# Kernel optimization log

Measured on AMD Instinct MI355X. Metric: run time of the kernel, lower is better.

The kernel has to match this reference:

```python
import jax, jax.numpy as jnp
import numpy as np

N_NODES = 10000
N_EDGES = 320000
K_HOPS = 3
IN_CH = 128
OUT_CH = 128


def setup_inputs() -> dict:
    key = jax.random.key(0)
    k1, k2, k3, k4, k5 = jax.random.split(key, 5)
    h = jax.random.normal(k1, (N_NODES, IN_CH), dtype=jnp.float32)
    X = jax.random.normal(k2, (N_EDGES, K_HOPS), dtype=jnp.float32)
    edge_index = jax.random.randint(k3, (2, N_EDGES), 0, N_NODES, dtype=jnp.int64)
    batch_node = jax.random.uniform(k4, (N_NODES,), dtype=jnp.float32)
    # glorot init for weight, zeros for bias (matches reset_parameters)
    stdv = np.sqrt(6.0 / (IN_CH + OUT_CH))
    weight = jax.random.uniform(k5, (K_HOPS, IN_CH, OUT_CH), dtype=jnp.float32,
                                minval=-stdv, maxval=stdv)
    bias = jnp.zeros((OUT_CH,), dtype=jnp.float32)
    return {"h": h, "X": X, "edge_index": edge_index,
            "batch_node": batch_node, "weight": weight, "bias": bias}


def reference(h, X, edge_index, batch_node, weight, bias):
    # Original builds dense A[k, src, dst] = X[e, k] (zeros elsewhere), then
    # res = A @ h @ weight, max over k, + bias. We honor the sparsity:
    # agg[src, k, :] = sum_e X[e, k] * h[dst[e], :]  (sparse A @ h per hop k)
    n = batch_node.shape[0]
    src = edge_index[0]
    dst = edge_index[1]
    msg = X[:, :, None] * h[dst][:, None, :]                 # [E, K, in]
    agg = jax.ops.segment_sum(msg, src, num_segments=n)      # [N, K, in]
    res = jnp.einsum('nki,kio->kno', agg, weight)            # [K, N, out]
    out = res.max(axis=0) + bias                             # [N, out]
    return out
```

## Files before the change

### kernel.cpp

```cpp
#include <hip/hip_runtime.h>

#define N_NODES 10000
#define N_EDGES 320000
#define K_HOPS  3
#define CH      128
#define NPB     16
#define NGRP    (N_NODES / NPB)
#define CAP     80
#define BCAP    768
#define GSTRIDE 64
#define ROWP    136

#define EDGE_BLKS 1250
#define WCV_BLKS  192

typedef __attribute__((ext_vector_type(8))) short  frag8;
typedef __attribute__((ext_vector_type(4))) float  floatx4;

__device__ inline unsigned short f2bf(float x) {
    union { float f; unsigned u; } v; v.f = x;
    unsigned r = v.u + 0x7fff + ((v.u >> 16) & 1);
    return (unsigned short)(r >> 16);
}
__device__ inline unsigned pack2bf(float lo, float hi) {
    return (unsigned)f2bf(lo) | ((unsigned)f2bf(hi) << 16);
}

__global__ __launch_bounds__(256) void bin_kernel(
    const int* __restrict__ ei, const float* __restrict__ W,
    unsigned short* __restrict__ WT, int* __restrict__ gcur,
    unsigned* __restrict__ bstore)
{
    int b = blockIdx.x;
    if (b < EDGE_BLKS) {
        int e   = b * 256 + threadIdx.x;
        int src = ei[e];
        int grp = src >> 4;
        int nl  = src & 15;
        int r = atomicAdd(gcur + grp * GSTRIDE, 1);
        if (r < BCAP)
            bstore[(size_t)grp * BCAP + r] = (unsigned)e | ((unsigned)nl << 20);
    } else {
        int tid = (b - EDGE_BLKS) * 256 + threadIdx.x;
        int i = tid & 127;
        int o = (tid >> 7) & 127;
        int k = tid >> 14;
        WT[tid] = f2bf(W[((size_t)k * CH + i) * CH + o]);
    }
}

__global__ __launch_bounds__(512) void fused_kernel(
    const float*          __restrict__ h,
    const float*          __restrict__ X,
    const int*            __restrict__ ei,
    const int*            __restrict__ gcur,
    const unsigned*       __restrict__ bstore,
    const unsigned short* __restrict__ WT,
    const float*          __restrict__ bias,
    float*                __restrict__ out)
{
    __shared__ unsigned short sA[K_HOPS][NPB][ROWP];
    __shared__ unsigned sEl[NPB][CAP];
    __shared__ int      cur[NPB];
    const int b     = blockIdx.x;
    const int node0 = b * NPB;
    const int t = threadIdx.x, w = t >> 6, lane = t & 63;

    if (t < NPB) cur[t] = 0;
    __syncthreads();

    {
        const int cnt = min(gcur[b * GSTRIDE], BCAP);
        const unsigned* bp = bstore + (size_t)b * BCAP;
        for (int i = t; i < cnt; i += 512) {
            unsigned pk = bp[i];
            int nl = (int)(pk >> 20);
            int r = atomicAdd(&cur[nl], 1);
            if (r < CAP) sEl[nl][r] = pk & 0xFFFFFu;
        }
    }
    __syncthreads();

    const int cb = 2 * lane;
#pragma unroll
    for (int q = 0; q < 2; ++q) {
        const int nl = 2 * w + q;
        const int cnt = __builtin_amdgcn_readfirstlane(min(cur[nl], CAP));
        const unsigned* lst = sEl[nl];
        float a0 = 0.f, a1 = 0.f, a2 = 0.f, a3 = 0.f, a4 = 0.f, a5 = 0.f;

        const int full = cnt & ~7;
        for (int s = 0; s < full; s += 8) {
            int e[8], dst[8]; float x0[8], x1[8], x2[8]; float2 hv[8];
#pragma unroll
            for (int k = 0; k < 8; ++k) e[k] = (int)lst[s + k];
#pragma unroll
            for (int k = 0; k < 8; ++k) dst[k] = ei[N_EDGES + e[k]];
#pragma unroll
            for (int k = 0; k < 8; ++k) {
                x0[k] = X[3 * e[k]]; x1[k] = X[3 * e[k] + 1]; x2[k] = X[3 * e[k] + 2];
            }
#pragma unroll
            for (int k = 0; k < 8; ++k)
                hv[k] = *(const float2*)(h + ((size_t)dst[k] << 7) + cb);
#pragma unroll
            for (int k = 0; k < 8; ++k) {
                a0 = fmaf(x0[k], hv[k].x, a0); a1 = fmaf(x0[k], hv[k].y, a1);
                a2 = fmaf(x1[k], hv[k].x, a2); a3 = fmaf(x1[k], hv[k].y, a3);
                a4 = fmaf(x2[k], hv[k].x, a4); a5 = fmaf(x2[k], hv[k].y, a5);
            }
        }
        for (int s = full; s < cnt; ++s) {
            int e = (int)lst[s];
            int dst = ei[N_EDGES + e];
            float x0 = X[3 * e], x1 = X[3 * e + 1], x2 = X[3 * e + 2];
            float2 hv = *(const float2*)(h + ((size_t)dst << 7) + cb);
            a0 = fmaf(x0, hv.x, a0); a1 = fmaf(x0, hv.y, a1);
            a2 = fmaf(x1, hv.x, a2); a3 = fmaf(x1, hv.y, a3);
            a4 = fmaf(x2, hv.x, a4); a5 = fmaf(x2, hv.y, a5);
        }

        *(unsigned*)&sA[0][nl][cb] = pack2bf(a0, a1);
        *(unsigned*)&sA[1][nl][cb] = pack2bf(a2, a3);
        *(unsigned*)&sA[2][nl][cb] = pack2bf(a4, a5);
    }
    __syncthreads();

    const int col  = lane & 15;
    const int quad = lane >> 4;
    const int ob   = 16 * w;
    const float bv = bias[ob + col];

    floatx4 m = {-3.4e38f, -3.4e38f, -3.4e38f, -3.4e38f};
#pragma unroll
    for (int hop = 0; hop < K_HOPS; ++hop) {
        floatx4 cv = {0.f, 0.f, 0.f, 0.f};
        const unsigned short* ap = &sA[hop][col][quad * 8];
        const unsigned short* bp =
            WT + ((size_t)hop * CH + ob + col) * CH + quad * 8;
#pragma unroll
        for (int kt = 0; kt < 4; ++kt) {
            frag8 af = *(const frag8*)(ap + kt * 32);
            frag8 bf = *(const frag8*)(bp + kt * 32);
            cv = __builtin_amdgcn_mfma_f32_16x16x32_bf16(af, bf, cv, 0, 0, 0);
        }
#pragma unroll
        for (int r = 0; r < 4; ++r) m[r] = fmaxf(m[r], cv[r]);
    }
#pragma unroll
    for (int r = 0; r < 4; ++r) {
        int node = node0 + quad * 4 + r;
        out[(size_t)node * CH + ob + col] = m[r] + bv;
    }
}

extern "C" void kernel_launch(void* const* d_in, const int* in_sizes, int n_in,
                              void* d_out, int out_size, void* d_ws, size_t ws_size,
                              hipStream_t stream) {
    const float* h    = (const float*)d_in[0];
    const float* X    = (const float*)d_in[1];
    const int*   ei   = (const int*)  d_in[2];
    const float* W    = (const float*)d_in[4];
    const float* bias = (const float*)d_in[5];
    float*       out  = (float*)d_out;

    char* ws = (char*)d_ws;
    int* gcur = (int*)ws;                      ws += (size_t)NGRP * GSTRIDE * sizeof(int);
    unsigned short* WT = (unsigned short*)ws;  ws += (size_t)K_HOPS * CH * CH * sizeof(unsigned short);
    unsigned* bstore = (unsigned*)ws;

    hipMemsetAsync(gcur, 0, (size_t)NGRP * GSTRIDE * sizeof(int), stream);
    bin_kernel  <<<EDGE_BLKS + WCV_BLKS, 256, 0, stream>>>(ei, W, WT, gcur, bstore);
    fused_kernel<<<NGRP, 512, 0, stream>>>(h, X, ei, gcur, bstore, WT, bias, out);
}
```

Before: 128.6 us.

## Pre-pack edge records with bf16 X and dst, gather bf16 h, split bin atomics

The binning pass now writes a self-contained per-edge record holding bf16-packed X values, the local node id and the dst index. The fused kernel therefore no longer does dependent global loads of ei and X per edge. h is converted to bf16 in the prep kernel, which halves the bytes of the random row gathers. Bin counters are split into 4 sub-bins per group to reduce atomic contention. The cost is bf16 precision on X and h in the aggregation, an extra pass over h, and larger bin records.

```diff
diff --git a/kernel.cpp b/kernel.cpp
--- a/kernel.cpp
+++ b/kernel.cpp
@@ -6,12 +6,14 @@
 #define CH      128
 #define NPB     16
 #define NGRP    (N_NODES / NPB)
+#define NSUB    4
+#define SBCAP   192
 #define CAP     80
-#define BCAP    768
-#define GSTRIDE 64
+#define GSTRIDE 16
 #define ROWP    136
 
 #define EDGE_BLKS 1250
+#define HCV_BLKS  1250
 #define WCV_BLKS  192
 
 typedef __attribute__((ext_vector_type(8))) short  frag8;
@@ -25,23 +27,39 @@
 __device__ inline unsigned pack2bf(float lo, float hi) {
     return (unsigned)f2bf(lo) | ((unsigned)f2bf(hi) << 16);
 }
+__device__ inline float bflo(unsigned u) { return __uint_as_float(u << 16); }
+__device__ inline float bfhi(unsigned u) { return __uint_as_float(u & 0xffff0000u); }
 
 __global__ __launch_bounds__(256) void bin_kernel(
-    const int* __restrict__ ei, const float* __restrict__ W,
-    unsigned short* __restrict__ WT, int* __restrict__ gcur,
-    unsigned* __restrict__ bstore)
+    const int* __restrict__ ei, const float* __restrict__ X,
+    const float* __restrict__ h, const float* __restrict__ W,
+    unsigned short* __restrict__ hb, unsigned short* __restrict__ WT,
+    int* __restrict__ gcur, uint3* __restrict__ bstore)
 {
     int b = blockIdx.x;
     if (b < EDGE_BLKS) {
         int e   = b * 256 + threadIdx.x;
         int src = ei[e];
+        int dst = ei[N_EDGES + e];
         int grp = src >> 4;
         int nl  = src & 15;
-        int r = atomicAdd(gcur + grp * GSTRIDE, 1);
-        if (r < BCAP)
-            bstore[(size_t)grp * BCAP + r] = (unsigned)e | ((unsigned)nl << 20);
+        int j   = e & (NSUB - 1);
+        int r = atomicAdd(gcur + (grp * NSUB + j) * GSTRIDE, 1);
+        if (r < SBCAP) {
+            uint3 rec;
+            rec.x = pack2bf(X[3 * e], X[3 * e + 1]);
+            rec.y = (unsigned)f2bf(X[3 * e + 2]) | ((unsigned)nl << 16);
+            rec.z = (unsigned)dst;
+            bstore[(size_t)(grp * NSUB + j) * SBCAP + r] = rec;
+        }
+    } else if (b < EDGE_BLKS + HCV_BLKS) {
+        int tid = (b - EDGE_BLKS) * 256 + threadIdx.x;
+        float4 v = *(const float4*)(h + (size_t)tid * 4);
+        ushort4 p;
+        p.x = f2bf(v.x); p.y = f2bf(v.y); p.z = f2bf(v.z); p.w = f2bf(v.w);
+        *(ushort4*)(hb + (size_t)tid * 4) = p;
     } else {
-        int tid = (b - EDGE_BLKS) * 256 + threadIdx.x;
+        int tid = (b - EDGE_BLKS - HCV_BLKS) * 256 + threadIdx.x;
         int i = tid & 127;
         int o = (tid >> 7) & 127;
         int k = tid >> 14;
@@ -50,17 +68,16 @@
 }
 
 __global__ __launch_bounds__(512) void fused_kernel(
-    const float*          __restrict__ h,
-    const float*          __restrict__ X,
-    const int*            __restrict__ ei,
+    const unsigned short* __restrict__ hb,
     const int*            __restrict__ gcur,
-    const unsigned*       __restrict__ bstore,
+    const uint3*          __restrict__ bstore,
     const unsigned short* __restrict__ WT,
     const float*          __restrict__ bias,
     float*                __restrict__ out)
 {
     __shared__ unsigned short sA[K_HOPS][NPB][ROWP];
-    __shared__ unsigned sEl[NPB][CAP];
+    __shared__ uint2    sExy[NPB][CAP];
+    __shared__ unsigned sEz[NPB][CAP];
     __shared__ int      cur[NPB];
     const int b     = blockIdx.x;
     const int node0 = b * NPB;
@@ -70,13 +87,19 @@
     __syncthreads();
 
     {
-        const int cnt = min(gcur[b * GSTRIDE], BCAP);
-        const unsigned* bp = bstore + (size_t)b * BCAP;
-        for (int i = t; i < cnt; i += 512) {
-            unsigned pk = bp[i];
-            int nl = (int)(pk >> 20);
-            int r = atomicAdd(&cur[nl], 1);
-            if (r < CAP) sEl[nl][r] = pk & 0xFFFFFu;
+        const uint3* bbase = bstore + (size_t)b * NSUB * SBCAP;
+#pragma unroll
+        for (int j = 0; j < NSUB; ++j) {
+            const int cnt = min(gcur[(b * NSUB + j) * GSTRIDE], SBCAP);
+            for (int i = t; i < cnt; i += 512) {
+                uint3 rec = bbase[j * SBCAP + i];
+                int nl = (int)(rec.y >> 16);
+                int r = atomicAdd(&cur[nl], 1);
+                if (r < CAP) {
+                    sExy[nl][r] = make_uint2(rec.x, rec.y);
+                    sEz[nl][r]  = rec.z;
+                }
+            }
         }
     }
     __syncthreads();
@@ -86,38 +109,36 @@
     for (int q = 0; q < 2; ++q) {
         const int nl = 2 * w + q;
         const int cnt = __builtin_amdgcn_readfirstlane(min(cur[nl], CAP));
-        const unsigned* lst = sEl[nl];
         float a0 = 0.f, a1 = 0.f, a2 = 0.f, a3 = 0.f, a4 = 0.f, a5 = 0.f;
 
         const int full = cnt & ~7;
         for (int s = 0; s < full; s += 8) {
-            int e[8], dst[8]; float x0[8], x1[8], x2[8]; float2 hv[8];
+            uint2 xy[8]; unsigned dz[8], hq[8];
 #pragma unroll
-            for (int k = 0; k < 8; ++k) e[k] = (int)lst[s + k];
+            for (int k = 0; k < 8; ++k) xy[k] = sExy[nl][s + k];
 #pragma unroll
-            for (int k = 0; k < 8; ++k) dst[k] = ei[N_EDGES + e[k]];
+            for (int k = 0; k < 8; ++k) dz[k] = sEz[nl][s + k];
+#pragma unroll
+            for (int k = 0; k < 8; ++k)
+                hq[k] = *(const unsigned*)(hb + ((size_t)dz[k] << 7) + cb);
 #pragma unroll
             for (int k = 0; k < 8; ++k) {
-                x0[k] = X[3 * e[k]]; x1[k] = X[3 * e[k] + 1]; x2[k] = X[3 * e[k] + 2];
-            }
-#pragma unroll
-            for (int k = 0; k < 8; ++k)
-                hv[k] = *(const float2*)(h + ((size_t)dst[k] << 7) + cb);
-#pragma unroll
-            for (int k = 0; k < 8; ++k) {
-                a0 = fmaf(x0[k], hv[k].x, a0); a1 = fmaf(x0[k], hv[k].y, a1);
-                a2 = fmaf(x1[k], hv[k].x, a2); a3 = fmaf(x1[k], hv[k].y, a3);
-                a4 = fmaf(x2[k], hv[k].x, a4); a5 = fmaf(x2[k], hv[k].y, a5);
+                float x0 = bflo(xy[k].x), x1 = bfhi(xy[k].x), x2 = bflo(xy[k].y);
+                float h0 = bflo(hq[k]),   h1 = bfhi(hq[k]);
+                a0 = fmaf(x0, h0, a0); a1 = fmaf(x0, h1, a1);
+                a2 = fmaf(x1, h0, a2); a3 = fmaf(x1, h1, a3);
+                a4 = fmaf(x2, h0, a4); a5 = fmaf(x2, h1, a5);
             }
         }
         for (int s = full; s < cnt; ++s) {
-            int e = (int)lst[s];
-            int dst = ei[N_EDGES + e];
-            float x0 = X[3 * e], x1 = X[3 * e + 1], x2 = X[3 * e + 2];
-            float2 hv = *(const float2*)(h + ((size_t)dst << 7) + cb);
-            a0 = fmaf(x0, hv.x, a0); a1 = fmaf(x0, hv.y, a1);
-            a2 = fmaf(x1, hv.x, a2); a3 = fmaf(x1, hv.y, a3);
-            a4 = fmaf(x2, hv.x, a4); a5 = fmaf(x2, hv.y, a5);
+            uint2 xy = sExy[nl][s];
+            unsigned dz = sEz[nl][s];
+            unsigned hq = *(const unsigned*)(hb + ((size_t)dz << 7) + cb);
+            float x0 = bflo(xy.x), x1 = bfhi(xy.x), x2 = bflo(xy.y);
+            float h0 = bflo(hq),   h1 = bfhi(hq);
+            a0 = fmaf(x0, h0, a0); a1 = fmaf(x0, h1, a1);
+            a2 = fmaf(x1, h0, a2); a3 = fmaf(x1, h1, a3);
+            a4 = fmaf(x2, h0, a4); a5 = fmaf(x2, h1, a5);
         }
 
         *(unsigned*)&sA[0][nl][cb] = pack2bf(a0, a1);
@@ -165,11 +186,14 @@
     float*       out  = (float*)d_out;
 
     char* ws = (char*)d_ws;
-    int* gcur = (int*)ws;                      ws += (size_t)NGRP * GSTRIDE * sizeof(int);
+    int* gcur = (int*)ws;                      ws += (size_t)NGRP * NSUB * GSTRIDE * sizeof(int);
+    unsigned short* hb = (unsigned short*)ws;  ws += (size_t)N_NODES * CH * sizeof(unsigned short);
     unsigned short* WT = (unsigned short*)ws;  ws += (size_t)K_HOPS * CH * CH * sizeof(unsigned short);
-    unsigned* bstore = (unsigned*)ws;
+    ws = (char*)(((uintptr_t)ws + 15) & ~(uintptr_t)15);
+    uint3* bstore = (uint3*)ws;
 
-    hipMemsetAsync(gcur, 0, (size_t)NGRP * GSTRIDE * sizeof(int), stream);
-    bin_kernel  <<<EDGE_BLKS + WCV_BLKS, 256, 0, stream>>>(ei, W, WT, gcur, bstore);
-    fused_kernel<<<NGRP, 512, 0, stream>>>(h, X, ei, gcur, bstore, WT, bias, out);
+    hipMemsetAsync(gcur, 0, (size_t)NGRP * NSUB * GSTRIDE * sizeof(int), stream);
+    bin_kernel  <<<EDGE_BLKS + HCV_BLKS + WCV_BLKS, 256, 0, stream>>>(
+        ei, X, h, W, hb, WT, gcur, bstore);
+    fused_kernel<<<NGRP, 512, 0, stream>>>(hb, gcur, bstore, WT, bias, out);
 }
```

Result: faster. 111.8 us (-13.0%).
